# Performance work log

Hardware: AMD Instinct MI355X
Metric: run time of the kernel (lower is better)

Reference implementation:

```python
import jax, jax.numpy as jnp
import numpy as np

N, E, B = 50000, 600000, 512
IN, HID, META = 128, 128, 27


def _gcn_layer(h_in, W, b, src, dst, norm, n_nodes):
    # GCNConv: out = scatter_add_{dst}( norm * (x W)[src] ) + b
    h = h_in @ W  # [N, HID]
    msg = h[src] * norm[:, None]  # [E+N, HID] gather + scale
    out = jax.ops.segment_sum(msg, dst, num_segments=n_nodes)
    return out + b


def setup_inputs() -> dict:
    key = jax.random.key(0)
    ks = jax.random.split(key, 16)
    x = jax.random.normal(ks[0], (N, IN), dtype=jnp.float32)
    edge_index = jax.random.randint(ks[1], (2, E), 0, N, dtype=jnp.int64)
    batch = jnp.sort(jax.random.randint(ks[2], (N,), 0, B, dtype=jnp.int64))
    metadata = jax.random.normal(ks[3], (B, META), dtype=jnp.float32)
    def glorot(k, shape):
        lim = np.sqrt(6.0 / (shape[0] + shape[1]))
        return jax.random.uniform(k, shape, jnp.float32, -lim, lim)
    params = {
        'W1': glorot(ks[4], (IN, HID)),  'b1': jnp.zeros((HID,), jnp.float32),
        'W2': glorot(ks[5], (HID, HID)), 'b2': jnp.zeros((HID,), jnp.float32),
        'W3': glorot(ks[6], (HID, HID)), 'b3': jnp.zeros((HID,), jnp.float32),
        'Wh1': glorot(ks[7], (HID + META, HID)), 'bh1': jnp.zeros((HID,), jnp.float32),
        'Wh2': glorot(ks[8], (HID, 1)),  'bh2': jnp.zeros((1,), jnp.float32),
    }
    return {'x': x, 'edge_index': edge_index, 'batch': batch, 'metadata': metadata, **params}


def reference(x, edge_index, batch, metadata, W1, b1, W2, b2, W3, b3, Wh1, bh1, Wh2, bh2):
    n_nodes = x.shape[0]
    # add self loops (PyG GCNConv default)
    loops = jnp.arange(n_nodes, dtype=edge_index.dtype)
    src = jnp.concatenate([edge_index[0], loops])
    dst = jnp.concatenate([edge_index[1], loops])
    # symmetric degree normalization D^{-1/2} A_hat D^{-1/2}
    deg = jax.ops.segment_sum(jnp.ones_like(dst, dtype=x.dtype), dst, num_segments=n_nodes)
    dinv = jax.lax.rsqrt(jnp.maximum(deg, 1.0))  # self-loops guarantee deg >= 1
    norm = dinv[src] * dinv[dst]  # [E+N]
    h = jax.nn.relu(_gcn_layer(x, W1, b1, src, dst, norm, n_nodes))
    h = jax.nn.relu(_gcn_layer(h, W2, b2, src, dst, norm, n_nodes))
    h = jax.nn.relu(_gcn_layer(h, W3, b3, src, dst, norm, n_nodes))
    # global mean pool over graphs
    n_graphs = metadata.shape[0]
    summed = jax.ops.segment_sum(h, batch, num_segments=n_graphs)  # [B, HID]
    counts = jax.ops.segment_sum(jnp.ones((n_nodes,), x.dtype), batch, num_segments=n_graphs)
    emb = summed / jnp.maximum(counts, 1.0)[:, None]
    # MLP head
    z = jnp.concatenate([emb, metadata], axis=1)  # [B, HID+META]
    z = jax.nn.relu(z @ Wh1 + bh1)
    return z @ Wh2 + bh2  # [B, 1] raw logits
```

## Files before the change

kernel.cpp:

```cpp
#include <hip/hip_runtime.h>

#define NN 50000
#define NE 600000
#define NB 512
#define HD 128
#define NMETA 27
#define SCAN_BLOCKS ((NN + 255) / 256)

typedef __attribute__((ext_vector_type(8))) short short8;
typedef __attribute__((ext_vector_type(4))) float f32x4;

__device__ __forceinline__ float relu(float x) { return fmaxf(x, 0.0f); }

__device__ __forceinline__ unsigned short f2bf(float f) {
    unsigned u = __float_as_uint(f);
    unsigned r = u + 0x7FFFu + ((u >> 16) & 1u);
    return (unsigned short)(r >> 16);
}
__device__ __forceinline__ float bf2f(unsigned short v) {
    return __uint_as_float(((unsigned)v) << 16);
}

__global__ __launch_bounds__(256) void k_count(const int* __restrict__ dst, int* __restrict__ cnt) {
    int i = blockIdx.x * 256 + threadIdx.x;
    if (i < NE) atomicAdd(&cnt[dst[i]], 1);
}

__global__ __launch_bounds__(256) void k_scanA(const int* __restrict__ cnt, int* __restrict__ partial,
                                               int* __restrict__ blocksum, float* __restrict__ dinv) {
    const int t = threadIdx.x;
    const int i = blockIdx.x * 256 + t;
    int v = (i < NN) ? cnt[i] : 0;
    if (i < NN) dinv[i] = rsqrtf((float)v + 1.0f);
    __shared__ int s[256];
    s[t] = v;
    __syncthreads();
    for (int off = 1; off < 256; off <<= 1) {
        int u = (t >= off) ? s[t - off] : 0;
        __syncthreads();
        s[t] += u;
        __syncthreads();
    }
    if (i < NN) partial[i] = s[t] - v;
    if (t == 255) blocksum[blockIdx.x] = s[255];
}

__global__ __launch_bounds__(256) void k_scanB(const int* __restrict__ blocksum, int* __restrict__ blockoff) {
    const int t = threadIdx.x;
    int v = (t < SCAN_BLOCKS) ? blocksum[t] : 0;
    __shared__ int s[256];
    s[t] = v;
    __syncthreads();
    for (int off = 1; off < 256; off <<= 1) {
        int u = (t >= off) ? s[t - off] : 0;
        __syncthreads();
        s[t] += u;
        __syncthreads();
    }
    if (t < SCAN_BLOCKS) blockoff[t] = s[t] - v;
}

__global__ __launch_bounds__(256) void k_scanC(const int* __restrict__ partial, const int* __restrict__ blockoff,
                                               int* __restrict__ rowptr, int* __restrict__ cursor) {
    const int i = blockIdx.x * 256 + threadIdx.x;
    if (i < NN) {
        int rp = partial[i] + blockoff[i >> 8];
        rowptr[i] = rp;
        cursor[i] = rp;
    }
    if (i == 0) rowptr[NN] = NE;
}

__global__ __launch_bounds__(256) void k_fill(const int* __restrict__ src, const int* __restrict__ dst,
                                              const float* __restrict__ dinv, int* __restrict__ cursor,
                                              int2* __restrict__ csr_sw) {
    int e = blockIdx.x * 256 + threadIdx.x;
    if (e >= NE) return;
    int s = src[e], d = dst[e];
    int pos = atomicAdd(&cursor[d], 1);
    csr_sw[pos] = make_int2(s, __float_as_int(dinv[s] * dinv[d]));
}

__global__ __launch_bounds__(256) void k_castWt3(const float* __restrict__ W1, const float* __restrict__ W2,
                                                 const float* __restrict__ W3, unsigned short* __restrict__ Wt1,
                                                 unsigned short* __restrict__ Wt2, unsigned short* __restrict__ Wt3) {
    int i = blockIdx.x * 256 + threadIdx.x;
    if (i >= 3 * HD * HD) return;
    int which = i / (HD * HD);
    int r = i - which * (HD * HD);
    int k = r >> 7, n = r & 127;
    const float* W = (which == 0) ? W1 : (which == 1) ? W2 : W3;
    unsigned short* Wt = (which == 0) ? Wt1 : (which == 1) ? Wt2 : Wt3;
    Wt[n * HD + k] = f2bf(W[r]);
}

__global__ __launch_bounds__(256) void k_gemm_x(const float* __restrict__ X,
                                                const unsigned short* __restrict__ Wt,
                                                unsigned short* __restrict__ T) {
    __shared__ unsigned short Ws[HD * HD];
    char* wsb = (char*)Ws;
    for (int i = threadIdx.x; i < HD * HD / 8; i += 256) {
        short8 v = ((const short8*)Wt)[i];
        int byte = i * 16;
        *(short8*)(wsb + (byte ^ (((byte >> 8) & 7) << 4))) = v;
    }
    __syncthreads();

    const int wave = threadIdx.x >> 6;
    const int lane = threadIdx.x & 63;
    const int lr = lane & 15;
    const int kh = lane >> 4;
    const int r0 = blockIdx.x * 64 + wave * 16;
    const float* arow = X + (size_t)min(r0 + lr, NN - 1) * HD + kh * 8;

    f32x4 acc[8] = {};
#pragma unroll
    for (int kk = 0; kk < 4; ++kk) {
        float4 a0 = *reinterpret_cast<const float4*>(arow + kk * 32);
        float4 a1 = *reinterpret_cast<const float4*>(arow + kk * 32 + 4);
        short8 af;
        af[0] = (short)f2bf(a0.x); af[1] = (short)f2bf(a0.y);
        af[2] = (short)f2bf(a0.z); af[3] = (short)f2bf(a0.w);
        af[4] = (short)f2bf(a1.x); af[5] = (short)f2bf(a1.y);
        af[6] = (short)f2bf(a1.z); af[7] = (short)f2bf(a1.w);
#pragma unroll
        for (int n = 0; n < 8; ++n) {
            int byte = (n * 16 + lr) * 256 + kk * 64 + kh * 16;
            short8 bf = *(const short8*)(wsb + (byte ^ (((byte >> 8) & 7) << 4)));
            acc[n] = __builtin_amdgcn_mfma_f32_16x16x32_bf16(af, bf, acc[n], 0, 0, 0);
        }
    }
#pragma unroll
    for (int n = 0; n < 8; ++n) {
#pragma unroll
        for (int r = 0; r < 4; ++r) {
            int row = r0 + kh * 4 + r;
            if (row < NN) T[(size_t)row * HD + n * 16 + lr] = f2bf(acc[n][r]);
        }
    }
}

template <int DO_GEMM>
__global__ __launch_bounds__(512, 8) void k_fused(const int* __restrict__ rowptr, const int2* __restrict__ csr_sw,
                                                  const unsigned short* __restrict__ Tin, const float* __restrict__ dinv,
                                                  const float* __restrict__ b, const unsigned short* __restrict__ Wt,
                                                  unsigned short* __restrict__ Out) {
    __shared__ unsigned short Hs[32 * HD];
    char* hsb = (char*)Hs;

    const int rl  = threadIdx.x >> 4;
    const int l16 = threadIdx.x & 15;
    const int row = blockIdx.x * 32 + rl;
    const int c0  = l16 * 4;
    const int c1  = 64 + l16 * 4;

    float a0x = 0.f, a0y = 0.f, a0z = 0.f, a0w = 0.f;
    float a1x = 0.f, a1y = 0.f, a1z = 0.f, a1w = 0.f;

    if (row < NN) {
        const int lo = rowptr[row], hi = rowptr[row + 1];
        int j = lo;
        int2 sA0, sA1, sA2, sA3, sB0, sB1, sB2, sB3;
        bool haveA = (j + 3 < hi);
        if (haveA) { sA0 = csr_sw[j]; sA1 = csr_sw[j + 1]; sA2 = csr_sw[j + 2]; sA3 = csr_sw[j + 3]; }
        while (haveA) {
            const int jn = j + 4;
            const bool haveB = (jn + 3 < hi);
            if (haveB) { sB0 = csr_sw[jn]; sB1 = csr_sw[jn + 1]; sB2 = csr_sw[jn + 2]; sB3 = csr_sw[jn + 3]; }
            const unsigned short* r0 = Tin + (size_t)sA0.x * HD;
            const unsigned short* r1 = Tin + (size_t)sA1.x * HD;
            const unsigned short* r2 = Tin + (size_t)sA2.x * HD;
            const unsigned short* r3 = Tin + (size_t)sA3.x * HD;
            ushort4 p00 = *reinterpret_cast<const ushort4*>(r0 + c0);
            ushort4 p01 = *reinterpret_cast<const ushort4*>(r0 + c1);
            ushort4 p10 = *reinterpret_cast<const ushort4*>(r1 + c0);
            ushort4 p11 = *reinterpret_cast<const ushort4*>(r1 + c1);
            ushort4 p20 = *reinterpret_cast<const ushort4*>(r2 + c0);
            ushort4 p21 = *reinterpret_cast<const ushort4*>(r2 + c1);
            ushort4 p30 = *reinterpret_cast<const ushort4*>(r3 + c0);
            ushort4 p31 = *reinterpret_cast<const ushort4*>(r3 + c1);
            float w0 = __int_as_float(sA0.y), w1 = __int_as_float(sA1.y);
            float w2 = __int_as_float(sA2.y), w3 = __int_as_float(sA3.y);
            a0x = fmaf(bf2f(p00.x), w0, a0x); a0y = fmaf(bf2f(p00.y), w0, a0y);
            a0z = fmaf(bf2f(p00.z), w0, a0z); a0w = fmaf(bf2f(p00.w), w0, a0w);
            a1x = fmaf(bf2f(p01.x), w0, a1x); a1y = fmaf(bf2f(p01.y), w0, a1y);
            a1z = fmaf(bf2f(p01.z), w0, a1z); a1w = fmaf(bf2f(p01.w), w0, a1w);
            a0x = fmaf(bf2f(p10.x), w1, a0x); a0y = fmaf(bf2f(p10.y), w1, a0y);
            a0z = fmaf(bf2f(p10.z), w1, a0z); a0w = fmaf(bf2f(p10.w), w1, a0w);
            a1x = fmaf(bf2f(p11.x), w1, a1x); a1y = fmaf(bf2f(p11.y), w1, a1y);
            a1z = fmaf(bf2f(p11.z), w1, a1z); a1w = fmaf(bf2f(p11.w), w1, a1w);
            a0x = fmaf(bf2f(p20.x), w2, a0x); a0y = fmaf(bf2f(p20.y), w2, a0y);
            a0z = fmaf(bf2f(p20.z), w2, a0z); a0w = fmaf(bf2f(p20.w), w2, a0w);
            a1x = fmaf(bf2f(p21.x), w2, a1x); a1y = fmaf(bf2f(p21.y), w2, a1y);
            a1z = fmaf(bf2f(p21.z), w2, a1z); a1w = fmaf(bf2f(p21.w), w2, a1w);
            a0x = fmaf(bf2f(p30.x), w3, a0x); a0y = fmaf(bf2f(p30.y), w3, a0y);
            a0z = fmaf(bf2f(p30.z), w3, a0z); a0w = fmaf(bf2f(p30.w), w3, a0w);
            a1x = fmaf(bf2f(p31.x), w3, a1x); a1y = fmaf(bf2f(p31.y), w3, a1y);
            a1z = fmaf(bf2f(p31.z), w3, a1z); a1w = fmaf(bf2f(p31.w), w3, a1w);
            j = jn;
            sA0 = sB0; sA1 = sB1; sA2 = sB2; sA3 = sB3;
            haveA = haveB;
        }
        for (; j < hi; ++j) {
            int2 sw = csr_sw[j];
            float w = __int_as_float(sw.y);
            const unsigned short* rr = Tin + (size_t)sw.x * HD;
            ushort4 t0 = *reinterpret_cast<const ushort4*>(rr + c0);
            ushort4 t1 = *reinterpret_cast<const ushort4*>(rr + c1);
            a0x = fmaf(bf2f(t0.x), w, a0x); a0y = fmaf(bf2f(t0.y), w, a0y);
            a0z = fmaf(bf2f(t0.z), w, a0z); a0w = fmaf(bf2f(t0.w), w, a0w);
            a1x = fmaf(bf2f(t1.x), w, a1x); a1y = fmaf(bf2f(t1.y), w, a1y);
            a1z = fmaf(bf2f(t1.z), w, a1z); a1w = fmaf(bf2f(t1.w), w, a1w);
        }
        const float di = dinv[row];
        const float sl = di * di;
        ushort4 ts0 = *reinterpret_cast<const ushort4*>(Tin + (size_t)row * HD + c0);
        ushort4 ts1 = *reinterpret_cast<const ushort4*>(Tin + (size_t)row * HD + c1);
        float4 bb0 = *reinterpret_cast<const float4*>(b + c0);
        float4 bb1 = *reinterpret_cast<const float4*>(b + c1);
        ushort4 o0, o1;
        o0.x = f2bf(relu(fmaf(bf2f(ts0.x), sl, a0x) + bb0.x));
        o0.y = f2bf(relu(fmaf(bf2f(ts0.y), sl, a0y) + bb0.y));
        o0.z = f2bf(relu(fmaf(bf2f(ts0.z), sl, a0z) + bb0.z));
        o0.w = f2bf(relu(fmaf(bf2f(ts0.w), sl, a0w) + bb0.w));
        o1.x = f2bf(relu(fmaf(bf2f(ts1.x), sl, a1x) + bb1.x));
        o1.y = f2bf(relu(fmaf(bf2f(ts1.y), sl, a1y) + bb1.y));
        o1.z = f2bf(relu(fmaf(bf2f(ts1.z), sl, a1z) + bb1.z));
        o1.w = f2bf(relu(fmaf(bf2f(ts1.w), sl, a1w) + bb1.w));
        if (DO_GEMM) {
            int byte0 = rl * 256 + c0 * 2;
            int byte1 = rl * 256 + c1 * 2;
            *(ushort4*)(hsb + (byte0 ^ (((byte0 >> 8) & 7) << 4))) = o0;
            *(ushort4*)(hsb + (byte1 ^ (((byte1 >> 8) & 7) << 4))) = o1;
        } else {
            *reinterpret_cast<ushort4*>(Out + (size_t)row * HD + c0) = o0;
            *reinterpret_cast<ushort4*>(Out + (size_t)row * HD + c1) = o1;
        }
    } else if (DO_GEMM) {
        ushort4 z = {0, 0, 0, 0};
        int byte0 = rl * 256 + c0 * 2;
        int byte1 = rl * 256 + c1 * 2;
        *(ushort4*)(hsb + (byte0 ^ (((byte0 >> 8) & 7) << 4))) = z;
        *(ushort4*)(hsb + (byte1 ^ (((byte1 >> 8) & 7) << 4))) = z;
    }

    if (DO_GEMM) {
        __syncthreads();
        const int w = threadIdx.x >> 6;
        const int lane = threadIdx.x & 63;
        const int lr = lane & 15;
        const int kh = lane >> 4;
        f32x4 acc0 = {}, acc1 = {};
#pragma unroll
        for (int kk = 0; kk < 4; ++kk) {
            short8 bf = *reinterpret_cast<const short8*>(Wt + (size_t)(w * 16 + lr) * HD + kk * 32 + kh * 8);
            int byteA = lr * 256 + kk * 64 + kh * 16;
            int byteB = (16 + lr) * 256 + kk * 64 + kh * 16;
            short8 af0 = *(const short8*)(hsb + (byteA ^ (((byteA >> 8) & 7) << 4)));
            short8 af1 = *(const short8*)(hsb + (byteB ^ (((byteB >> 8) & 7) << 4)));
            acc0 = __builtin_amdgcn_mfma_f32_16x16x32_bf16(af0, bf, acc0, 0, 0, 0);
            acc1 = __builtin_amdgcn_mfma_f32_16x16x32_bf16(af1, bf, acc1, 0, 0, 0);
        }
#pragma unroll
        for (int r = 0; r < 4; ++r) {
            int row0 = blockIdx.x * 32 + kh * 4 + r;
            int row1 = row0 + 16;
            if (row0 < NN) Out[(size_t)row0 * HD + w * 16 + lr] = f2bf(acc0[r]);
            if (row1 < NN) Out[(size_t)row1 * HD + w * 16 + lr] = f2bf(acc1[r]);
        }
    }
}

__global__ __launch_bounds__(128) void k_poolhead(const unsigned short* __restrict__ H, const int* __restrict__ batch,
                                                  const float* __restrict__ meta,
                                                  const float* __restrict__ Wh1, const float* __restrict__ bh1,
                                                  const float* __restrict__ Wh2, const float* __restrict__ bh2,
                                                  float* __restrict__ out) {
    int g = blockIdx.x;
    int l = 0, r = NN;
    while (l < r) { int m = (l + r) >> 1; if (batch[m] < g) l = m + 1; else r = m; }
    int lo = l;
    r = NN;
    while (l < r) { int m = (l + r) >> 1; if (batch[m] < g + 1) l = m + 1; else r = m; }
    int hi = l;
    int c = threadIdx.x;
    float s = 0.0f;
    for (int i = lo; i < hi; ++i) s += bf2f(H[(size_t)i * HD + c]);
    float cnt = (float)max(hi - lo, 1);
    __shared__ float emb[128];
    emb[c] = s / cnt;
    __syncthreads();
    float z = bh1[c];
    for (int k = 0; k < HD; ++k) z = fmaf(emb[k], Wh1[k * HD + c], z);
    for (int k = 0; k < NMETA; ++k) z = fmaf(meta[g * NMETA + k], Wh1[(HD + k) * HD + c], z);
    z = relu(z);
    __shared__ float red[128];
    red[c] = z * Wh2[c];
    __syncthreads();
    for (int st = 64; st > 0; st >>= 1) {
        if (c < st) red[c] += red[c + st];
        __syncthreads();
    }
    if (c == 0) out[g] = red[0] + bh2[0];
}

extern "C" void kernel_launch(void* const* d_in, const int* in_sizes, int n_in,
                              void* d_out, int out_size, void* d_ws, size_t ws_size,
                              hipStream_t stream) {
    const float* x     = (const float*)d_in[0];
    const int*   ei    = (const int*)d_in[1];
    const int*   src   = ei;
    const int*   dst   = ei + NE;
    const int*   batch = (const int*)d_in[2];
    const float* meta  = (const float*)d_in[3];
    const float* W1 = (const float*)d_in[4];  const float* b1 = (const float*)d_in[5];
    const float* W2 = (const float*)d_in[6];  const float* b2 = (const float*)d_in[7];
    const float* W3 = (const float*)d_in[8];  const float* b3 = (const float*)d_in[9];
    const float* Wh1 = (const float*)d_in[10]; const float* bh1 = (const float*)d_in[11];
    const float* Wh2 = (const float*)d_in[12]; const float* bh2 = (const float*)d_in[13];
    float* out = (float*)d_out;

    int2*  csr_sw   = (int2*)d_ws;
    int*   cnt      = (int*)(csr_sw + NE);
    int*   partial  = cnt + NN;
    int*   blocksum = partial + NN;
    int*   blockoff = blocksum + 256;
    int*   rowptr   = blockoff + 256;
    int*   cursor   = rowptr + NN + 8;
    float* dinv     = (float*)(cursor + NN);
    unsigned short* Ta  = (unsigned short*)(dinv + NN);
    unsigned short* Tc  = Ta + (size_t)NN * HD;
    unsigned short* Hb  = Tc + (size_t)NN * HD;
    unsigned short* Wt1 = Hb + (size_t)NN * HD;
    unsigned short* Wt2 = Wt1 + HD * HD;
    unsigned short* Wt3 = Wt2 + HD * HD;

    const int GEMM_GRID  = (NN + 63) / 64;
    const int FUSED_GRID = (NN + 31) / 32;
    const int CWT_GRID   = (3 * HD * HD + 255) / 256;

    hipMemsetAsync(cnt, 0, NN * sizeof(int), stream);
    k_count<<<(NE + 255) / 256, 256, 0, stream>>>(dst, cnt);
    k_scanA<<<SCAN_BLOCKS, 256, 0, stream>>>(cnt, partial, blocksum, dinv);
    k_scanB<<<1, 256, 0, stream>>>(blocksum, blockoff);
    k_scanC<<<SCAN_BLOCKS, 256, 0, stream>>>(partial, blockoff, rowptr, cursor);
    k_fill<<<(NE + 255) / 256, 256, 0, stream>>>(src, dst, dinv, cursor, csr_sw);

    k_castWt3<<<CWT_GRID, 256, 0, stream>>>(W1, W2, W3, Wt1, Wt2, Wt3);

    k_gemm_x<<<GEMM_GRID, 256, 0, stream>>>(x, Wt1, Ta);
    k_fused<1><<<FUSED_GRID, 512, 0, stream>>>(rowptr, csr_sw, Ta, dinv, b1, Wt2, Tc);
    k_fused<1><<<FUSED_GRID, 512, 0, stream>>>(rowptr, csr_sw, Tc, dinv, b2, Wt3, Ta);
    k_fused<0><<<FUSED_GRID, 512, 0, stream>>>(rowptr, csr_sw, Ta, dinv, b3, (const unsigned short*)nullptr, Hb);

    k_poolhead<<<NB, 128, 0, stream>>>(Hb, batch, meta, Wh1, bh1, Wh2, bh2, out);
}
```

Before: 322.4 us.

## Pre-scale features by dinv, drop edge weights, fuse mean-pool into last layer

Refactors the normalization so each GEMM output row is pre-multiplied by dinv[src] and the aggregation multiplies by dinv[dst] once per row. This lets the CSR store only source indices, halving the edge-array traffic and replacing per-edge FMAs with adds. The final GCN layer now keeps its fp32 output in shared memory and atomically adds per-graph partial sums into an embedding buffer. That removes the bf16 H write and the serial pooling scan in the head kernel. It adds atomics and a memset, and changes rounding slightly because bf16 storage now holds pre-scaled values.

```diff
diff --git a/kernel.cpp b/kernel.cpp
--- a/kernel.cpp
+++ b/kernel.cpp
@@ -72,13 +72,12 @@
 }
 
 __global__ __launch_bounds__(256) void k_fill(const int* __restrict__ src, const int* __restrict__ dst,
-                                              const float* __restrict__ dinv, int* __restrict__ cursor,
-                                              int2* __restrict__ csr_sw) {
+                                              int* __restrict__ cursor, int* __restrict__ csr_src) {
     int e = blockIdx.x * 256 + threadIdx.x;
     if (e >= NE) return;
     int s = src[e], d = dst[e];
     int pos = atomicAdd(&cursor[d], 1);
-    csr_sw[pos] = make_int2(s, __float_as_int(dinv[s] * dinv[d]));
+    csr_src[pos] = s;
 }
 
 __global__ __launch_bounds__(256) void k_castWt3(const float* __restrict__ W1, const float* __restrict__ W2,
@@ -96,6 +95,7 @@
 
 __global__ __launch_bounds__(256) void k_gemm_x(const float* __restrict__ X,
                                                 const unsigned short* __restrict__ Wt,
+                                                const float* __restrict__ dinv,
                                                 unsigned short* __restrict__ T) {
     __shared__ unsigned short Ws[HD * HD];
     char* wsb = (char*)Ws;
@@ -130,23 +130,32 @@
             acc[n] = __builtin_amdgcn_mfma_f32_16x16x32_bf16(af, bf, acc[n], 0, 0, 0);
         }
     }
+    float dv[4];
+#pragma unroll
+    for (int r = 0; r < 4; ++r) {
+        int row = r0 + kh * 4 + r;
+        dv[r] = (row < NN) ? dinv[row] : 0.0f;
+    }
 #pragma unroll
     for (int n = 0; n < 8; ++n) {
 #pragma unroll
         for (int r = 0; r < 4; ++r) {
             int row = r0 + kh * 4 + r;
-            if (row < NN) T[(size_t)row * HD + n * 16 + lr] = f2bf(acc[n][r]);
-        }
-    }
-}
-
-template <int DO_GEMM>
-__global__ __launch_bounds__(512, 8) void k_fused(const int* __restrict__ rowptr, const int2* __restrict__ csr_sw,
+            if (row < NN) T[(size_t)row * HD + n * 16 + lr] = f2bf(acc[n][r] * dv[r]);
+        }
+    }
+}
+
+template <int MODE>
+__global__ __launch_bounds__(512, 8) void k_fused(const int* __restrict__ rowptr, const int* __restrict__ csr_src,
                                                   const unsigned short* __restrict__ Tin, const float* __restrict__ dinv,
                                                   const float* __restrict__ b, const unsigned short* __restrict__ Wt,
-                                                  unsigned short* __restrict__ Out) {
-    __shared__ unsigned short Hs[32 * HD];
-    char* hsb = (char*)Hs;
+                                                  unsigned short* __restrict__ Out, const int* __restrict__ batch,
+                                                  float* __restrict__ embsum) {
+    __shared__ char smem[32 * 132 * 4 + 128];
+    char* hsb = smem;
+    float* hsf = (float*)smem;
+    int* sg = (int*)(smem + 32 * 132 * 4);
 
     const int rl  = threadIdx.x >> 4;
     const int l16 = threadIdx.x & 15;
@@ -154,23 +163,28 @@
     const int c0  = l16 * 4;
     const int c1  = 64 + l16 * 4;
 
+    if (MODE == 2 && threadIdx.x < 32) {
+        int rr = blockIdx.x * 32 + threadIdx.x;
+        sg[threadIdx.x] = (rr < NN) ? batch[rr] : -1;
+    }
+
     float a0x = 0.f, a0y = 0.f, a0z = 0.f, a0w = 0.f;
     float a1x = 0.f, a1y = 0.f, a1z = 0.f, a1w = 0.f;
 
     if (row < NN) {
         const int lo = rowptr[row], hi = rowptr[row + 1];
         int j = lo;
-        int2 sA0, sA1, sA2, sA3, sB0, sB1, sB2, sB3;
+        int sA0, sA1, sA2, sA3, sB0, sB1, sB2, sB3;
         bool haveA = (j + 3 < hi);
-        if (haveA) { sA0 = csr_sw[j]; sA1 = csr_sw[j + 1]; sA2 = csr_sw[j + 2]; sA3 = csr_sw[j + 3]; }
+        if (haveA) { sA0 = csr_src[j]; sA1 = csr_src[j + 1]; sA2 = csr_src[j + 2]; sA3 = csr_src[j + 3]; }
         while (haveA) {
             const int jn = j + 4;
             const bool haveB = (jn + 3 < hi);
-            if (haveB) { sB0 = csr_sw[jn]; sB1 = csr_sw[jn + 1]; sB2 = csr_sw[jn + 2]; sB3 = csr_sw[jn + 3]; }
-            const unsigned short* r0 = Tin + (size_t)sA0.x * HD;
-            const unsigned short* r1 = Tin + (size_t)sA1.x * HD;
-            const unsigned short* r2 = Tin + (size_t)sA2.x * HD;
-            const unsigned short* r3 = Tin + (size_t)sA3.x * HD;
+            if (haveB) { sB0 = csr_src[jn]; sB1 = csr_src[jn + 1]; sB2 = csr_src[jn + 2]; sB3 = csr_src[jn + 3]; }
+            const unsigned short* r0 = Tin + (size_t)sA0 * HD;
+            const unsigned short* r1 = Tin + (size_t)sA1 * HD;
+            const unsigned short* r2 = Tin + (size_t)sA2 * HD;
+            const unsigned short* r3 = Tin + (size_t)sA3 * HD;
             ushort4 p00 = *reinterpret_cast<const ushort4*>(r0 + c0);
             ushort4 p01 = *reinterpret_cast<const ushort4*>(r0 + c1);
             ushort4 p10 = *reinterpret_cast<const ushort4*>(r1 + c0);
@@ -179,73 +193,67 @@
             ushort4 p21 = *reinterpret_cast<const ushort4*>(r2 + c1);
             ushort4 p30 = *reinterpret_cast<const ushort4*>(r3 + c0);
             ushort4 p31 = *reinterpret_cast<const ushort4*>(r3 + c1);
-            float w0 = __int_as_float(sA0.y), w1 = __int_as_float(sA1.y);
-            float w2 = __int_as_float(sA2.y), w3 = __int_as_float(sA3.y);
-            a0x = fmaf(bf2f(p00.x), w0, a0x); a0y = fmaf(bf2f(p00.y), w0, a0y);
-            a0z = fmaf(bf2f(p00.z), w0, a0z); a0w = fmaf(bf2f(p00.w), w0, a0w);
-            a1x = fmaf(bf2f(p01.x), w0, a1x); a1y = fmaf(bf2f(p01.y), w0, a1y);
-            a1z = fmaf(bf2f(p01.z), w0, a1z); a1w = fmaf(bf2f(p01.w), w0, a1w);
-            a0x = fmaf(bf2f(p10.x), w1, a0x); a0y = fmaf(bf2f(p10.y), w1, a0y);
-            a0z = fmaf(bf2f(p10.z), w1, a0z); a0w = fmaf(bf2f(p10.w), w1, a0w);
-            a1x = fmaf(bf2f(p11.x), w1, a1x); a1y = fmaf(bf2f(p11.y), w1, a1y);
-            a1z = fmaf(bf2f(p11.z), w1, a1z); a1w = fmaf(bf2f(p11.w), w1, a1w);
-            a0x = fmaf(bf2f(p20.x), w2, a0x); a0y = fmaf(bf2f(p20.y), w2, a0y);
-            a0z = fmaf(bf2f(p20.z), w2, a0z); a0w = fmaf(bf2f(p20.w), w2, a0w);
-            a1x = fmaf(bf2f(p21.x), w2, a1x); a1y = fmaf(bf2f(p21.y), w2, a1y);
-            a1z = fmaf(bf2f(p21.z), w2, a1z); a1w = fmaf(bf2f(p21.w), w2, a1w);
-            a0x = fmaf(bf2f(p30.x), w3, a0x); a0y = fmaf(bf2f(p30.y), w3, a0y);
-            a0z = fmaf(bf2f(p30.z), w3, a0z); a0w = fmaf(bf2f(p30.w), w3, a0w);
-            a1x = fmaf(bf2f(p31.x), w3, a1x); a1y = fmaf(bf2f(p31.y), w3, a1y);
-            a1z = fmaf(bf2f(p31.z), w3, a1z); a1w = fmaf(bf2f(p31.w), w3, a1w);
+            a0x += bf2f(p00.x); a0y += bf2f(p00.y); a0z += bf2f(p00.z); a0w += bf2f(p00.w);
+            a1x += bf2f(p01.x); a1y += bf2f(p01.y); a1z += bf2f(p01.z); a1w += bf2f(p01.w);
+            a0x += bf2f(p10.x); a0y += bf2f(p10.y); a0z += bf2f(p10.z); a0w += bf2f(p10.w);
+            a1x += bf2f(p11.x); a1y += bf2f(p11.y); a1z += bf2f(p11.z); a1w += bf2f(p11.w);
+            a0x += bf2f(p20.x); a0y += bf2f(p20.y); a0z += bf2f(p20.z); a0w += bf2f(p20.w);
+            a1x += bf2f(p21.x); a1y += bf2f(p21.y); a1z += bf2f(p21.z); a1w += bf2f(p21.w);
+            a0x += bf2f(p30.x); a0y += bf2f(p30.y); a0z += bf2f(p30.z); a0w += bf2f(p30.w);
+            a1x += bf2f(p31.x); a1y += bf2f(p31.y); a1z += bf2f(p31.z); a1w += bf2f(p31.w);
             j = jn;
             sA0 = sB0; sA1 = sB1; sA2 = sB2; sA3 = sB3;
             haveA = haveB;
         }
         for (; j < hi; ++j) {
-            int2 sw = csr_sw[j];
-            float w = __int_as_float(sw.y);
-            const unsigned short* rr = Tin + (size_t)sw.x * HD;
+            int s = csr_src[j];
+            const unsigned short* rr = Tin + (size_t)s * HD;
             ushort4 t0 = *reinterpret_cast<const ushort4*>(rr + c0);
             ushort4 t1 = *reinterpret_cast<const ushort4*>(rr + c1);
-            a0x = fmaf(bf2f(t0.x), w, a0x); a0y = fmaf(bf2f(t0.y), w, a0y);
-            a0z = fmaf(bf2f(t0.z), w, a0z); a0w = fmaf(bf2f(t0.w), w, a0w);
-            a1x = fmaf(bf2f(t1.x), w, a1x); a1y = fmaf(bf2f(t1.y), w, a1y);
-            a1z = fmaf(bf2f(t1.z), w, a1z); a1w = fmaf(bf2f(t1.w), w, a1w);
+            a0x += bf2f(t0.x); a0y += bf2f(t0.y); a0z += bf2f(t0.z); a0w += bf2f(t0.w);
+            a1x += bf2f(t1.x); a1y += bf2f(t1.y); a1z += bf2f(t1.z); a1w += bf2f(t1.w);
         }
         const float di = dinv[row];
-        const float sl = di * di;
         ushort4 ts0 = *reinterpret_cast<const ushort4*>(Tin + (size_t)row * HD + c0);
         ushort4 ts1 = *reinterpret_cast<const ushort4*>(Tin + (size_t)row * HD + c1);
         float4 bb0 = *reinterpret_cast<const float4*>(b + c0);
         float4 bb1 = *reinterpret_cast<const float4*>(b + c1);
-        ushort4 o0, o1;
-        o0.x = f2bf(relu(fmaf(bf2f(ts0.x), sl, a0x) + bb0.x));
-        o0.y = f2bf(relu(fmaf(bf2f(ts0.y), sl, a0y) + bb0.y));
-        o0.z = f2bf(relu(fmaf(bf2f(ts0.z), sl, a0z) + bb0.z));
-        o0.w = f2bf(relu(fmaf(bf2f(ts0.w), sl, a0w) + bb0.w));
-        o1.x = f2bf(relu(fmaf(bf2f(ts1.x), sl, a1x) + bb1.x));
-        o1.y = f2bf(relu(fmaf(bf2f(ts1.y), sl, a1y) + bb1.y));
-        o1.z = f2bf(relu(fmaf(bf2f(ts1.z), sl, a1z) + bb1.z));
-        o1.w = f2bf(relu(fmaf(bf2f(ts1.w), sl, a1w) + bb1.w));
-        if (DO_GEMM) {
+        float h0x = relu(fmaf(di, a0x + bf2f(ts0.x), bb0.x));
+        float h0y = relu(fmaf(di, a0y + bf2f(ts0.y), bb0.y));
+        float h0z = relu(fmaf(di, a0z + bf2f(ts0.z), bb0.z));
+        float h0w = relu(fmaf(di, a0w + bf2f(ts0.w), bb0.w));
+        float h1x = relu(fmaf(di, a1x + bf2f(ts1.x), bb1.x));
+        float h1y = relu(fmaf(di, a1y + bf2f(ts1.y), bb1.y));
+        float h1z = relu(fmaf(di, a1z + bf2f(ts1.z), bb1.z));
+        float h1w = relu(fmaf(di, a1w + bf2f(ts1.w), bb1.w));
+        if (MODE == 1) {
+            ushort4 o0, o1;
+            o0.x = f2bf(h0x); o0.y = f2bf(h0y); o0.z = f2bf(h0z); o0.w = f2bf(h0w);
+            o1.x = f2bf(h1x); o1.y = f2bf(h1y); o1.z = f2bf(h1z); o1.w = f2bf(h1w);
             int byte0 = rl * 256 + c0 * 2;
             int byte1 = rl * 256 + c1 * 2;
             *(ushort4*)(hsb + (byte0 ^ (((byte0 >> 8) & 7) << 4))) = o0;
             *(ushort4*)(hsb + (byte1 ^ (((byte1 >> 8) & 7) << 4))) = o1;
         } else {
-            *reinterpret_cast<ushort4*>(Out + (size_t)row * HD + c0) = o0;
-            *reinterpret_cast<ushort4*>(Out + (size_t)row * HD + c1) = o1;
-        }
-    } else if (DO_GEMM) {
-        ushort4 z = {0, 0, 0, 0};
-        int byte0 = rl * 256 + c0 * 2;
-        int byte1 = rl * 256 + c1 * 2;
-        *(ushort4*)(hsb + (byte0 ^ (((byte0 >> 8) & 7) << 4))) = z;
-        *(ushort4*)(hsb + (byte1 ^ (((byte1 >> 8) & 7) << 4))) = z;
-    }
-
-    if (DO_GEMM) {
-        __syncthreads();
+            *(float4*)(smem + (rl * 132 + c0) * 4) = make_float4(h0x, h0y, h0z, h0w);
+            *(float4*)(smem + (rl * 132 + c1) * 4) = make_float4(h1x, h1y, h1z, h1w);
+        }
+    } else {
+        if (MODE == 1) {
+            ushort4 z = {0, 0, 0, 0};
+            int byte0 = rl * 256 + c0 * 2;
+            int byte1 = rl * 256 + c1 * 2;
+            *(ushort4*)(hsb + (byte0 ^ (((byte0 >> 8) & 7) << 4))) = z;
+            *(ushort4*)(hsb + (byte1 ^ (((byte1 >> 8) & 7) << 4))) = z;
+        } else {
+            float4 z = make_float4(0.f, 0.f, 0.f, 0.f);
+            *(float4*)(smem + (rl * 132 + c0) * 4) = z;
+            *(float4*)(smem + (rl * 132 + c1) * 4) = z;
+        }
+    }
+    __syncthreads();
+
+    if (MODE == 1) {
         const int w = threadIdx.x >> 6;
         const int lane = threadIdx.x & 63;
         const int lr = lane & 15;
@@ -265,36 +273,62 @@
         for (int r = 0; r < 4; ++r) {
             int row0 = blockIdx.x * 32 + kh * 4 + r;
             int row1 = row0 + 16;
-            if (row0 < NN) Out[(size_t)row0 * HD + w * 16 + lr] = f2bf(acc0[r]);
-            if (row1 < NN) Out[(size_t)row1 * HD + w * 16 + lr] = f2bf(acc1[r]);
-        }
-    }
-}
-
-__global__ __launch_bounds__(128) void k_poolhead(const unsigned short* __restrict__ H, const int* __restrict__ batch,
-                                                  const float* __restrict__ meta,
-                                                  const float* __restrict__ Wh1, const float* __restrict__ bh1,
-                                                  const float* __restrict__ Wh2, const float* __restrict__ bh2,
-                                                  float* __restrict__ out) {
+            if (row0 < NN) Out[(size_t)row0 * HD + w * 16 + lr] = f2bf(acc0[r] * dinv[row0]);
+            if (row1 < NN) Out[(size_t)row1 * HD + w * 16 + lr] = f2bf(acc1[r] * dinv[row1]);
+        }
+    } else {
+        if (threadIdx.x < HD) {
+            const int c = threadIdx.x;
+            float acc = 0.f;
+            int gcur = -1;
+#pragma unroll 8
+            for (int r = 0; r < 32; ++r) {
+                int g = sg[r];
+                if (g != gcur) {
+                    if (gcur >= 0) atomicAdd(&embsum[gcur * HD + c], acc);
+                    acc = 0.f;
+                    gcur = g;
+                }
+                acc += hsf[r * 132 + c];
+            }
+            if (gcur >= 0) atomicAdd(&embsum[gcur * HD + c], acc);
+        }
+    }
+}
+
+__global__ __launch_bounds__(128) void k_head(const float* __restrict__ embsum, const int* __restrict__ batch,
+                                              const float* __restrict__ meta,
+                                              const float* __restrict__ Wh1, const float* __restrict__ bh1,
+                                              const float* __restrict__ Wh2, const float* __restrict__ bh2,
+                                              float* __restrict__ out) {
     int g = blockIdx.x;
+    int c = threadIdx.x;
     int l = 0, r = NN;
     while (l < r) { int m = (l + r) >> 1; if (batch[m] < g) l = m + 1; else r = m; }
     int lo = l;
     r = NN;
     while (l < r) { int m = (l + r) >> 1; if (batch[m] < g + 1) l = m + 1; else r = m; }
     int hi = l;
-    int c = threadIdx.x;
-    float s = 0.0f;
-    for (int i = lo; i < hi; ++i) s += bf2f(H[(size_t)i * HD + c]);
-    float cnt = (float)max(hi - lo, 1);
-    __shared__ float emb[128];
-    emb[c] = s / cnt;
-    __syncthreads();
+    float rcp = 1.0f / (float)max(hi - lo, 1);
+
+    __shared__ float emb[HD];
+    __shared__ float mt[NMETA];
+    emb[c] = embsum[g * HD + c] * rcp;
+    if (c < NMETA) mt[c] = meta[g * NMETA + c];
+    __syncthreads();
+
     float z = bh1[c];
-    for (int k = 0; k < HD; ++k) z = fmaf(emb[k], Wh1[k * HD + c], z);
-    for (int k = 0; k < NMETA; ++k) z = fmaf(meta[g * NMETA + k], Wh1[(HD + k) * HD + c], z);
+    float z0 = 0.f, z1 = 0.f, z2 = 0.f, z3 = 0.f;
+    for (int k = 0; k < HD; k += 4) {
+        z0 = fmaf(emb[k],     Wh1[k * HD + c],       z0);
+        z1 = fmaf(emb[k + 1], Wh1[(k + 1) * HD + c], z1);
+        z2 = fmaf(emb[k + 2], Wh1[(k + 2) * HD + c], z2);
+        z3 = fmaf(emb[k + 3], Wh1[(k + 3) * HD + c], z3);
+    }
+    for (int k = 0; k < NMETA; ++k) z = fmaf(mt[k], Wh1[(HD + k) * HD + c], z);
+    z += (z0 + z1) + (z2 + z3);
     z = relu(z);
-    __shared__ float red[128];
+    __shared__ float red[HD];
     red[c] = z * Wh2[c];
     __syncthreads();
     for (int st = 64; st > 0; st >>= 1) {
@@ -320,18 +354,18 @@
     const float* Wh2 = (const float*)d_in[12]; const float* bh2 = (const float*)d_in[13];
     float* out = (float*)d_out;
 
-    int2*  csr_sw   = (int2*)d_ws;
-    int*   cnt      = (int*)(csr_sw + NE);
+    int*   csr_src  = (int*)d_ws;
+    int*   cnt      = csr_src + NE;
     int*   partial  = cnt + NN;
     int*   blocksum = partial + NN;
     int*   blockoff = blocksum + 256;
     int*   rowptr   = blockoff + 256;
     int*   cursor   = rowptr + NN + 8;
     float* dinv     = (float*)(cursor + NN);
-    unsigned short* Ta  = (unsigned short*)(dinv + NN);
+    float* embsum   = dinv + NN;
+    unsigned short* Ta  = (unsigned short*)(embsum + NB * HD);
     unsigned short* Tc  = Ta + (size_t)NN * HD;
-    unsigned short* Hb  = Tc + (size_t)NN * HD;
-    unsigned short* Wt1 = Hb + (size_t)NN * HD;
+    unsigned short* Wt1 = Tc + (size_t)NN * HD;
     unsigned short* Wt2 = Wt1 + HD * HD;
     unsigned short* Wt3 = Wt2 + HD * HD;
 
@@ -340,18 +374,19 @@
     const int CWT_GRID   = (3 * HD * HD + 255) / 256;
 
     hipMemsetAsync(cnt, 0, NN * sizeof(int), stream);
+    hipMemsetAsync(embsum, 0, NB * HD * sizeof(float), stream);
     k_count<<<(NE + 255) / 256, 256, 0, stream>>>(dst, cnt);
     k_scanA<<<SCAN_BLOCKS, 256, 0, stream>>>(cnt, partial, blocksum, dinv);
     k_scanB<<<1, 256, 0, stream>>>(blocksum, blockoff);
     k_scanC<<<SCAN_BLOCKS, 256, 0, stream>>>(partial, blockoff, rowptr, cursor);
-    k_fill<<<(NE + 255) / 256, 256, 0, stream>>>(src, dst, dinv, cursor, csr_sw);
+    k_fill<<<(NE + 255) / 256, 256, 0, stream>>>(src, dst, cursor, csr_src);
 
     k_castWt3<<<CWT_GRID, 256, 0, stream>>>(W1, W2, W3, Wt1, Wt2, Wt3);
 
-    k_gemm_x<<<GEMM_GRID, 256, 0, stream>>>(x, Wt1, Ta);
-    k_fused<1><<<FUSED_GRID, 512, 0, stream>>>(rowptr, csr_sw, Ta, dinv, b1, Wt2, Tc);
-    k_fused<1><<<FUSED_GRID, 512, 0, stream>>>(rowptr, csr_sw, Tc, dinv, b2, Wt3, Ta);
-    k_fused<0><<<FUSED_GRID, 512, 0, stream>>>(rowptr, csr_sw, Ta, dinv, b3, (const unsigned short*)nullptr, Hb);
-
-    k_poolhead<<<NB, 128, 0, stream>>>(Hb, batch, meta, Wh1, bh1, Wh2, bh2, out);
-}
+    k_gemm_x<<<GEMM_GRID, 256, 0, stream>>>(x, Wt1, dinv, Ta);
+    k_fused<1><<<FUSED_GRID, 512, 0, stream>>>(rowptr, csr_src, Ta, dinv, b1, Wt2, Tc, nullptr, nullptr);
+    k_fused<1><<<FUSED_GRID, 512, 0, stream>>>(rowptr, csr_src, Tc, dinv, b2, Wt3, Ta, nullptr, nullptr);
+    k_fused<2><<<FUSED_GRID, 512, 0, stream>>>(rowptr, csr_src, Ta, dinv, b3, nullptr, nullptr, batch, embsum);
+
+    k_head<<<NB, 128, 0, stream>>>(embsum, batch, meta, Wh1, bh1, Wh2, bh2, out);
+}
```

Result: faster. 299.9 us (-7.0%).
